# Kernel tuning notes

Hardware: AMD Instinct MI355X
Metric: run time of the kernel (lower is better)

## Reference

```python
import jax, jax.numpy as jnp
import numpy as np


def setup_inputs() -> dict:
    key = jax.random.key(0)
    k1, k2, k3, k4 = jax.random.split(key, 4)
    N, E, C_in, C_out = 50000, 625000, 256, 128
    x = jax.random.normal(k1, (N, C_in), dtype=jnp.float32)
    W = jax.random.normal(k2, (C_out, C_in), dtype=jnp.float32) * (1.0 / np.sqrt(C_in))
    b = jax.random.normal(k3, (C_out,), dtype=jnp.float32) * 0.01
    edge_index = jax.random.randint(k4, (2, E), 0, N, dtype=jnp.int64)
    return {"x": x, "W": W, "b": b, "edge_index": edge_index}


def reference(x, W, b, edge_index):
    # x: [N, C_in], W: [C_out, C_in], b: [C_out], edge_index: [2, E]
    N = x.shape[0]
    h = jnp.dot(x, W.T) + b  # [N, C_out] (nn.Linear)
    r, c = edge_index[0], edge_index[1]
    # node degree via scatter_add of ones over destination index r
    deg = jax.ops.segment_sum(jnp.ones(r.shape[0], dtype=h.dtype), r, num_segments=N)
    # rsqrt with inf (deg==0) replaced by 0
    nd_rsqrt = jnp.where(deg > 0, jax.lax.rsqrt(jnp.maximum(deg, 1.0)), jnp.zeros_like(deg))
    # gather messages from source nodes c, normalize by source rsqrt-degree
    message_norm = h[c] * nd_rsqrt[c][:, None]  # [E, C_out]
    # scatter-add to destination nodes r
    out = jax.ops.segment_sum(message_norm, r, num_segments=N)  # [N, C_out]
    # final destination-side normalization
    return out * nd_rsqrt[:, None]
```

## Files before the change

### kernel.cpp

```cpp
#include <hip/hip_runtime.h>

#define C_IN 256
#define C_OUT 128
#define ELL_PAD 64
#define NBUCKMAX 512
#define BNODE 128
#define BUCK_CAP 2048
#define EDGES_PER_BLK 4096
#define BLK 128

typedef __attribute__((ext_vector_type(8))) short bf16x8;
typedef __attribute__((ext_vector_type(8))) unsigned short ushort8;
typedef __attribute__((ext_vector_type(4))) float f32x4;

__device__ inline unsigned short f2bf(float f) {
    unsigned u = __builtin_bit_cast(unsigned, f);
    unsigned r = (u + 0x7FFFu + ((u >> 16) & 1u)) >> 16;
    return (unsigned short)r;
}
__device__ inline float bflo(unsigned u) { return __builtin_bit_cast(float, u << 16); }
__device__ inline float bfhi(unsigned u) { return __builtin_bit_cast(float, u & 0xFFFF0000u); }

__global__ __launch_bounds__(BLK) void wconv_zero_kernel(const float* __restrict__ W,
                                                         unsigned short* __restrict__ WB,
                                                         int* __restrict__ bucket_cnt) {
    int ci = blockIdx.x * BLK + threadIdx.x;
    int q = ci & 3, cl = (ci >> 2) & 15, ctt = ci >> 6;
    int colw = (ctt & 7) * 16 + cl;
    int k0 = (ctt >> 3) * 32 + q * 8;
    const float* src = W + colw * C_IN + k0;
    bf16x8 o;
    #pragma unroll
    for (int j = 0; j < 8; ++j) o[j] = (short)f2bf(src[j]);
    *(bf16x8*)(WB + (size_t)ci * 8) = o;
    if (ci < NBUCKMAX) bucket_cnt[ci] = 0;
}

__global__ __launch_bounds__(BLK) void fused_bucket_gemm(const float* __restrict__ x,
                                                         const unsigned short* __restrict__ WB,
                                                         const float* __restrict__ b,
                                                         const int* __restrict__ ridx,
                                                         const int* __restrict__ cidx,
                                                         int* __restrict__ bucket_cnt,
                                                         unsigned* __restrict__ buckets,
                                                         unsigned short* __restrict__ h,
                                                         int N, int E, int nbuck, int G_bkt) {
    __shared__ unsigned stage[EDGES_PER_BLK];
    __shared__ int cnt[NBUCKMAX];
    __shared__ int base[NBUCKMAX];
    __shared__ int off[NBUCKMAX];
    int t = threadIdx.x;

    int T = gridDim.x;
    long long i = blockIdx.x;
    int f_i  = (int)((i * (long long)G_bkt) / T);
    int f_i1 = (int)(((i + 1) * (long long)G_bkt) / T);

    if (f_i1 > f_i) {
        int e0 = f_i * EDGES_PER_BLK;
        int nv = E - e0; if (nv > EDGES_PER_BLK) nv = EDGES_PER_BLK;

        for (int bb = t; bb < NBUCKMAX; bb += BLK) { cnt[bb] = 0; off[bb] = 0; }
        __syncthreads();

        for (int k = t; k < nv; k += BLK) {
            int r = ridx[e0 + k];
            int c = cidx[e0 + k];
            stage[k] = ((unsigned)r << 16) | (unsigned)c;
            atomicAdd(&cnt[r >> 7], 1);
        }
        __syncthreads();

        for (int bb = t; bb < nbuck; bb += BLK) {
            int cb = cnt[bb];
            base[bb] = (cb > 0) ? atomicAdd(&bucket_cnt[bb], cb) : 0;
        }
        __syncthreads();

        for (int k = t; k < nv; k += BLK) {
            unsigned v = stage[k];
            int bkt = (int)(v >> 23);
            int p = atomicAdd(&off[bkt], 1);
            int dst = base[bkt] + p;
            if (dst < BUCK_CAP)
                buckets[(size_t)bkt * BUCK_CAP + dst] = v;
        }
        return;
    }

    int gemmId = (int)i - f_i;
    int w = t >> 6, l = t & 63;
    int row0 = gemmId * 32;
    int lq = l >> 4, lr = l & 15;

    int arow = row0 + w * 16 + lr;
    bool rowok = (arow < N);
    const float* xr = x + (size_t)(rowok ? arow : 0) * C_IN + lq * 8;
    const char* wb = (const char*)WB;
    int boff = lr * 64 + lq * 16;

    f32x4 acc[8];
    #pragma unroll
    for (int ct = 0; ct < 8; ++ct) acc[ct] = (f32x4){0.f, 0.f, 0.f, 0.f};

    #pragma unroll
    for (int tt = 0; tt < 8; ++tt) {
        float4 v0 = make_float4(0.f, 0.f, 0.f, 0.f);
        float4 v1 = make_float4(0.f, 0.f, 0.f, 0.f);
        if (rowok) {
            v0 = *(const float4*)(xr + tt * 32);
            v1 = *(const float4*)(xr + tt * 32 + 4);
        }
        bf16x8 af;
        af[0] = (short)f2bf(v0.x); af[1] = (short)f2bf(v0.y);
        af[2] = (short)f2bf(v0.z); af[3] = (short)f2bf(v0.w);
        af[4] = (short)f2bf(v1.x); af[5] = (short)f2bf(v1.y);
        af[6] = (short)f2bf(v1.z); af[7] = (short)f2bf(v1.w);
        #pragma unroll
        for (int ct = 0; ct < 8; ++ct) {
            bf16x8 bfv = *(const bf16x8*)(wb + (tt * 8 + ct) * 1024 + boff);
            acc[ct] = __builtin_amdgcn_mfma_f32_16x16x32_bf16(af, bfv, acc[ct], 0, 0, 0);
        }
    }

    #pragma unroll
    for (int ct = 0; ct < 8; ++ct) {
        int colc = ct * 16 + lr;
        float bv = b[colc];
        #pragma unroll
        for (int r = 0; r < 4; ++r) {
            int grow = row0 + w * 16 + lq * 4 + r;
            if (grow < N)
                h[(size_t)grow * C_OUT + colc] = f2bf(acc[ct][r] + bv);
        }
    }
}

__global__ __launch_bounds__(BLK) void build_ell_kernel(const int* __restrict__ bucket_cnt,
                                                        const unsigned* __restrict__ buckets,
                                                        int* __restrict__ deg,
                                                        float* __restrict__ s,
                                                        unsigned short* __restrict__ col_ell, int N) {
    __shared__ int cur[BNODE];
    __shared__ unsigned short ell[BNODE * ELL_PAD];
    int t = threadIdx.x;
    int b = blockIdx.x;
    cur[t] = 0;
    __syncthreads();

    int cnt = bucket_cnt[b];
    if (cnt > BUCK_CAP) cnt = BUCK_CAP;
    const unsigned* bb = buckets + (size_t)b * BUCK_CAP;
    for (int e = t; e < cnt; e += BLK) {
        unsigned v = bb[e];
        int rl = (v >> 16) & (BNODE - 1);
        int pos = atomicAdd(&cur[rl], 1);
        if (pos < ELL_PAD)
            ell[rl * ELL_PAD + pos] = (unsigned short)(v & 0xFFFFu);
    }
    __syncthreads();

    int node = b * BNODE + t;
    if (node < N) {
        int d = cur[t];
        deg[node] = d;
        s[node] = (d > 0) ? rsqrtf((float)d) : 0.0f;
        if (d > ELL_PAD) d = ELL_PAD;
        int chunks = (d + 7) >> 3;
        ushort8* dst = (ushort8*)(col_ell + (size_t)node * ELL_PAD);
        const ushort8* src = (const ushort8*)(ell + t * ELL_PAD);
        for (int j = 0; j < chunks; ++j) dst[j] = src[j];
    }
}

__global__ __launch_bounds__(BLK) void gather_kernel(const int* __restrict__ deg,
                                                     const float* __restrict__ s,
                                                     const unsigned short* __restrict__ col_ell,
                                                     const unsigned short* __restrict__ h,
                                                     float* __restrict__ out, int N) {
    int gid = blockIdx.x * BLK + threadIdx.x;
    int node = gid >> 4;
    if (node >= N) return;
    int lane = gid & 15;

    int d = deg[node];
    float sv = s[node];
    int dd = (d > ELL_PAD) ? ELL_PAD : d;
    const unsigned short* cl = col_ell + (size_t)node * ELL_PAD;
    const char* hb = (const char*)h;

    float acc[8] = {0.f, 0.f, 0.f, 0.f, 0.f, 0.f, 0.f, 0.f};
    int i = 0;
    for (; i + 4 <= dd; i += 4) {
        int c0 = cl[i], c1 = cl[i + 1], c2 = cl[i + 2], c3 = cl[i + 3];
        float s0 = s[c0], s1 = s[c1], s2 = s[c2], s3 = s[c3];
        uint4 v0 = *(const uint4*)(hb + (size_t)c0 * (C_OUT * 2) + lane * 16);
        uint4 v1 = *(const uint4*)(hb + (size_t)c1 * (C_OUT * 2) + lane * 16);
        uint4 v2 = *(const uint4*)(hb + (size_t)c2 * (C_OUT * 2) + lane * 16);
        uint4 v3 = *(const uint4*)(hb + (size_t)c3 * (C_OUT * 2) + lane * 16);
        acc[0] += s0 * bflo(v0.x); acc[1] += s0 * bfhi(v0.x);
        acc[2] += s0 * bflo(v0.y); acc[3] += s0 * bfhi(v0.y);
        acc[4] += s0 * bflo(v0.z); acc[5] += s0 * bfhi(v0.z);
        acc[6] += s0 * bflo(v0.w); acc[7] += s0 * bfhi(v0.w);
        acc[0] += s1 * bflo(v1.x); acc[1] += s1 * bfhi(v1.x);
        acc[2] += s1 * bflo(v1.y); acc[3] += s1 * bfhi(v1.y);
        acc[4] += s1 * bflo(v1.z); acc[5] += s1 * bfhi(v1.z);
        acc[6] += s1 * bflo(v1.w); acc[7] += s1 * bfhi(v1.w);
        acc[0] += s2 * bflo(v2.x); acc[1] += s2 * bfhi(v2.x);
        acc[2] += s2 * bflo(v2.y); acc[3] += s2 * bfhi(v2.y);
        acc[4] += s2 * bflo(v2.z); acc[5] += s2 * bfhi(v2.z);
        acc[6] += s2 * bflo(v2.w); acc[7] += s2 * bfhi(v2.w);
        acc[0] += s3 * bflo(v3.x); acc[1] += s3 * bfhi(v3.x);
        acc[2] += s3 * bflo(v3.y); acc[3] += s3 * bfhi(v3.y);
        acc[4] += s3 * bflo(v3.z); acc[5] += s3 * bfhi(v3.z);
        acc[6] += s3 * bflo(v3.w); acc[7] += s3 * bfhi(v3.w);
    }
    for (; i < dd; ++i) {
        int c0 = cl[i];
        float s0 = s[c0];
        uint4 v0 = *(const uint4*)(hb + (size_t)c0 * (C_OUT * 2) + lane * 16);
        acc[0] += s0 * bflo(v0.x); acc[1] += s0 * bfhi(v0.x);
        acc[2] += s0 * bflo(v0.y); acc[3] += s0 * bfhi(v0.y);
        acc[4] += s0 * bflo(v0.z); acc[5] += s0 * bfhi(v0.z);
        acc[6] += s0 * bflo(v0.w); acc[7] += s0 * bfhi(v0.w);
    }
    float4 o0 = make_float4(acc[0] * sv, acc[1] * sv, acc[2] * sv, acc[3] * sv);
    float4 o1 = make_float4(acc[4] * sv, acc[5] * sv, acc[6] * sv, acc[7] * sv);
    float* op = out + (size_t)node * C_OUT + lane * 8;
    *(float4*)(op)     = o0;
    *(float4*)(op + 4) = o1;
}

extern "C" void kernel_launch(void* const* d_in, const int* in_sizes, int n_in,
                              void* d_out, int out_size, void* d_ws, size_t ws_size,
                              hipStream_t stream) {
    const float* x = (const float*)d_in[0];
    const float* W = (const float*)d_in[1];
    const float* b = (const float*)d_in[2];
    const int*   ei = (const int*)d_in[3];
    float* out = (float*)d_out;

    int N = in_sizes[0] / C_IN;
    int E = in_sizes[3] / 2;
    const int* ridx = ei;
    const int* cidx = ei + E;

    int nbuck = (N + BNODE - 1) / BNODE;

    char* wsc = (char*)d_ws;
    unsigned short* h  = (unsigned short*)wsc;       wsc += (size_t)N * C_OUT * sizeof(unsigned short);
    unsigned short* WB = (unsigned short*)wsc;       wsc += (size_t)C_OUT * C_IN * sizeof(unsigned short);
    int*   deg      = (int*)wsc;                     wsc += (size_t)N * sizeof(int);
    float* s        = (float*)wsc;                   wsc += (size_t)N * sizeof(float);
    unsigned short* col_ell = (unsigned short*)wsc;  wsc += (size_t)N * ELL_PAD * sizeof(unsigned short);
    int*   bucket_cnt = (int*)wsc;                   wsc += (size_t)NBUCKMAX * sizeof(int);
    unsigned* buckets = (unsigned*)wsc;

    wconv_zero_kernel<<<4096 / BLK, BLK, 0, stream>>>(W, WB, bucket_cnt);

    int G_bkt  = (E + EDGES_PER_BLK - 1) / EDGES_PER_BLK;
    int G_gemm = (N + 31) / 32;
    fused_bucket_gemm<<<G_bkt + G_gemm, BLK, 0, stream>>>(x, WB, b, ridx, cidx,
                                                          bucket_cnt, buckets, h,
                                                          N, E, nbuck, G_bkt);

    build_ell_kernel<<<nbuck, BLK, 0, stream>>>(bucket_cnt, buckets, deg, s, col_ell, N);

    long long gth = (long long)N * 16;
    gather_kernel<<<(int)((gth + BLK - 1) / BLK), BLK, 0, stream>>>(deg, s, col_ell, h, out, N);
}
```

Before: 71.18 us.

## Split GEMM across bucket and ELL-build kernels; coalesce bucket writes via local sort

```diff
diff --git a/kernel.cpp b/kernel.cpp
--- a/kernel.cpp
+++ b/kernel.cpp
@@ -20,6 +20,57 @@
 }
 __device__ inline float bflo(unsigned u) { return __builtin_bit_cast(float, u << 16); }
 __device__ inline float bfhi(unsigned u) { return __builtin_bit_cast(float, u & 0xFFFF0000u); }
+
+__device__ __forceinline__ void gemm_unit(int gemmId, const float* __restrict__ x,
+                                          const unsigned short* __restrict__ WB,
+                                          const float* __restrict__ b,
+                                          unsigned short* __restrict__ h, int N, int t) {
+    int w = t >> 6, l = t & 63;
+    int row0 = gemmId * 32;
+    int lq = l >> 4, lr = l & 15;
+
+    int arow = row0 + w * 16 + lr;
+    bool rowok = (arow < N);
+    const float* xr = x + (size_t)(rowok ? arow : 0) * C_IN + lq * 8;
+    const char* wb = (const char*)WB;
+    int boff = lr * 64 + lq * 16;
+
+    f32x4 acc[8];
+    #pragma unroll
+    for (int ct = 0; ct < 8; ++ct) acc[ct] = (f32x4){0.f, 0.f, 0.f, 0.f};
+
+    #pragma unroll
+    for (int tt = 0; tt < 8; ++tt) {
+        float4 v0 = make_float4(0.f, 0.f, 0.f, 0.f);
+        float4 v1 = make_float4(0.f, 0.f, 0.f, 0.f);
+        if (rowok) {
+            v0 = *(const float4*)(xr + tt * 32);
+            v1 = *(const float4*)(xr + tt * 32 + 4);
+        }
+        bf16x8 af;
+        af[0] = (short)f2bf(v0.x); af[1] = (short)f2bf(v0.y);
+        af[2] = (short)f2bf(v0.z); af[3] = (short)f2bf(v0.w);
+        af[4] = (short)f2bf(v1.x); af[5] = (short)f2bf(v1.y);
+        af[6] = (short)f2bf(v1.z); af[7] = (short)f2bf(v1.w);
+        #pragma unroll
+        for (int ct = 0; ct < 8; ++ct) {
+            bf16x8 bfv = *(const bf16x8*)(wb + (tt * 8 + ct) * 1024 + boff);
+            acc[ct] = __builtin_amdgcn_mfma_f32_16x16x32_bf16(af, bfv, acc[ct], 0, 0, 0);
+        }
+    }
+
+    #pragma unroll
+    for (int ct = 0; ct < 8; ++ct) {
+        int colc = ct * 16 + lr;
+        float bv = b[colc];
+        #pragma unroll
+        for (int r = 0; r < 4; ++r) {
+            int grow = row0 + w * 16 + lq * 4 + r;
+            if (grow < N)
+                h[(size_t)grow * C_OUT + colc] = f2bf(acc[ct][r] + bv);
+        }
+    }
+}
 
 __global__ __launch_bounds__(BLK) void wconv_zero_kernel(const float* __restrict__ W,
                                                          unsigned short* __restrict__ WB,
@@ -36,19 +87,22 @@
     if (ci < NBUCKMAX) bucket_cnt[ci] = 0;
 }
 
-__global__ __launch_bounds__(BLK) void fused_bucket_gemm(const float* __restrict__ x,
-                                                         const unsigned short* __restrict__ WB,
-                                                         const float* __restrict__ b,
-                                                         const int* __restrict__ ridx,
-                                                         const int* __restrict__ cidx,
-                                                         int* __restrict__ bucket_cnt,
-                                                         unsigned* __restrict__ buckets,
-                                                         unsigned short* __restrict__ h,
-                                                         int N, int E, int nbuck, int G_bkt) {
+__global__ __launch_bounds__(BLK) void k1_bucket_gemm(const float* __restrict__ x,
+                                                      const unsigned short* __restrict__ WB,
+                                                      const float* __restrict__ b,
+                                                      const int* __restrict__ ridx,
+                                                      const int* __restrict__ cidx,
+                                                      int* __restrict__ bucket_cnt,
+                                                      unsigned* __restrict__ buckets,
+                                                      unsigned short* __restrict__ h,
+                                                      int N, int E, int nbuck, int G_bkt) {
     __shared__ unsigned stage[EDGES_PER_BLK];
+    __shared__ unsigned stage2[EDGES_PER_BLK];
     __shared__ int cnt[NBUCKMAX];
-    __shared__ int base[NBUCKMAX];
+    __shared__ int lbase[NBUCKMAX];
+    __shared__ int gbase[NBUCKMAX];
     __shared__ int off[NBUCKMAX];
+    __shared__ int part[BLK];
     int t = threadIdx.x;
 
     int T = gridDim.x;
@@ -60,6 +114,7 @@
         int e0 = f_i * EDGES_PER_BLK;
         int nv = E - e0; if (nv > EDGES_PER_BLK) nv = EDGES_PER_BLK;
 
+        #pragma unroll
         for (int bb = t; bb < NBUCKMAX; bb += BLK) { cnt[bb] = 0; off[bb] = 0; }
         __syncthreads();
 
@@ -71,9 +126,24 @@
         }
         __syncthreads();
 
-        for (int bb = t; bb < nbuck; bb += BLK) {
+        int c0 = cnt[4 * t], c1 = cnt[4 * t + 1], c2 = cnt[4 * t + 2], c3 = cnt[4 * t + 3];
+        part[t] = c0 + c1 + c2 + c3;
+        __syncthreads();
+        for (int o = 1; o < BLK; o <<= 1) {
+            int v = (t >= o) ? part[t - o] : 0;
+            __syncthreads();
+            part[t] += v;
+            __syncthreads();
+        }
+        int ex = (t > 0) ? part[t - 1] : 0;
+        lbase[4 * t]     = ex;
+        lbase[4 * t + 1] = ex + c0;
+        lbase[4 * t + 2] = ex + c0 + c1;
+        lbase[4 * t + 3] = ex + c0 + c1 + c2;
+        #pragma unroll
+        for (int bb = t; bb < NBUCKMAX; bb += BLK) {
             int cb = cnt[bb];
-            base[bb] = (cb > 0) ? atomicAdd(&bucket_cnt[bb], cb) : 0;
+            gbase[bb] = (cb > 0) ? atomicAdd(&bucket_cnt[bb], cb) : 0;
         }
         __syncthreads();
 
@@ -81,96 +151,74 @@
             unsigned v = stage[k];
             int bkt = (int)(v >> 23);
             int p = atomicAdd(&off[bkt], 1);
-            int dst = base[bkt] + p;
-            if (dst < BUCK_CAP)
-                buckets[(size_t)bkt * BUCK_CAP + dst] = v;
+            stage2[lbase[bkt] + p] = v;
+        }
+        __syncthreads();
+
+        for (int k = t; k < nv; k += BLK) {
+            unsigned v = stage2[k];
+            int bkt = (int)(v >> 23);
+            int gofs = gbase[bkt] + (k - lbase[bkt]);
+            if (gofs < BUCK_CAP)
+                buckets[(size_t)bkt * BUCK_CAP + gofs] = v;
         }
         return;
     }
 
-    int gemmId = (int)i - f_i;
-    int w = t >> 6, l = t & 63;
-    int row0 = gemmId * 32;
-    int lq = l >> 4, lr = l & 15;
-
-    int arow = row0 + w * 16 + lr;
-    bool rowok = (arow < N);
-    const float* xr = x + (size_t)(rowok ? arow : 0) * C_IN + lq * 8;
-    const char* wb = (const char*)WB;
-    int boff = lr * 64 + lq * 16;
-
-    f32x4 acc[8];
-    #pragma unroll
-    for (int ct = 0; ct < 8; ++ct) acc[ct] = (f32x4){0.f, 0.f, 0.f, 0.f};
-
-    #pragma unroll
-    for (int tt = 0; tt < 8; ++tt) {
-        float4 v0 = make_float4(0.f, 0.f, 0.f, 0.f);
-        float4 v1 = make_float4(0.f, 0.f, 0.f, 0.f);
-        if (rowok) {
-            v0 = *(const float4*)(xr + tt * 32);
-            v1 = *(const float4*)(xr + tt * 32 + 4);
-        }
-        bf16x8 af;
-        af[0] = (short)f2bf(v0.x); af[1] = (short)f2bf(v0.y);
-        af[2] = (short)f2bf(v0.z); af[3] = (short)f2bf(v0.w);
-        af[4] = (short)f2bf(v1.x); af[5] = (short)f2bf(v1.y);
-        af[6] = (short)f2bf(v1.z); af[7] = (short)f2bf(v1.w);
-        #pragma unroll
-        for (int ct = 0; ct < 8; ++ct) {
-            bf16x8 bfv = *(const bf16x8*)(wb + (tt * 8 + ct) * 1024 + boff);
-            acc[ct] = __builtin_amdgcn_mfma_f32_16x16x32_bf16(af, bfv, acc[ct], 0, 0, 0);
-        }
-    }
-
-    #pragma unroll
-    for (int ct = 0; ct < 8; ++ct) {
-        int colc = ct * 16 + lr;
-        float bv = b[colc];
-        #pragma unroll
-        for (int r = 0; r < 4; ++r) {
-            int grow = row0 + w * 16 + lq * 4 + r;
-            if (grow < N)
-                h[(size_t)grow * C_OUT + colc] = f2bf(acc[ct][r] + bv);
-        }
-    }
-}
-
-__global__ __launch_bounds__(BLK) void build_ell_kernel(const int* __restrict__ bucket_cnt,
-                                                        const unsigned* __restrict__ buckets,
-                                                        int* __restrict__ deg,
-                                                        float* __restrict__ s,
-                                                        unsigned short* __restrict__ col_ell, int N) {
+    gemm_unit((int)i - f_i, x, WB, b, h, N, t);
+}
+
+__global__ __launch_bounds__(BLK) void k2_build_gemm(const float* __restrict__ x,
+                                                     const unsigned short* __restrict__ WB,
+                                                     const float* __restrict__ b,
+                                                     const int* __restrict__ bucket_cnt,
+                                                     const unsigned* __restrict__ buckets,
+                                                     int* __restrict__ deg,
+                                                     float* __restrict__ s,
+                                                     unsigned short* __restrict__ col_ell,
+                                                     unsigned short* __restrict__ h,
+                                                     int N, int nbuck, int G1) {
     __shared__ int cur[BNODE];
     __shared__ unsigned short ell[BNODE * ELL_PAD];
     int t = threadIdx.x;
-    int b = blockIdx.x;
-    cur[t] = 0;
-    __syncthreads();
-
-    int cnt = bucket_cnt[b];
-    if (cnt > BUCK_CAP) cnt = BUCK_CAP;
-    const unsigned* bb = buckets + (size_t)b * BUCK_CAP;
-    for (int e = t; e < cnt; e += BLK) {
-        unsigned v = bb[e];
-        int rl = (v >> 16) & (BNODE - 1);
-        int pos = atomicAdd(&cur[rl], 1);
-        if (pos < ELL_PAD)
-            ell[rl * ELL_PAD + pos] = (unsigned short)(v & 0xFFFFu);
-    }
-    __syncthreads();
-
-    int node = b * BNODE + t;
-    if (node < N) {
-        int d = cur[t];
-        deg[node] = d;
-        s[node] = (d > 0) ? rsqrtf((float)d) : 0.0f;
-        if (d > ELL_PAD) d = ELL_PAD;
-        int chunks = (d + 7) >> 3;
-        ushort8* dst = (ushort8*)(col_ell + (size_t)node * ELL_PAD);
-        const ushort8* src = (const ushort8*)(ell + t * ELL_PAD);
-        for (int j = 0; j < chunks; ++j) dst[j] = src[j];
-    }
+
+    int T = gridDim.x;
+    long long i = blockIdx.x;
+    int f_i  = (int)((i * (long long)nbuck) / T);
+    int f_i1 = (int)(((i + 1) * (long long)nbuck) / T);
+
+    if (f_i1 > f_i) {
+        int bkt = f_i;
+        cur[t] = 0;
+        __syncthreads();
+
+        int cnt = bucket_cnt[bkt];
+        if (cnt > BUCK_CAP) cnt = BUCK_CAP;
+        const unsigned* bb = buckets + (size_t)bkt * BUCK_CAP;
+        for (int e = t; e < cnt; e += BLK) {
+            unsigned v = bb[e];
+            int rl = (v >> 16) & (BNODE - 1);
+            int pos = atomicAdd(&cur[rl], 1);
+            if (pos < ELL_PAD)
+                ell[rl * ELL_PAD + pos] = (unsigned short)(v & 0xFFFFu);
+        }
+        __syncthreads();
+
+        int node = bkt * BNODE + t;
+        if (node < N) {
+            int d = cur[t];
+            deg[node] = d;
+            s[node] = (d > 0) ? rsqrtf((float)d) : 0.0f;
+            if (d > ELL_PAD) d = ELL_PAD;
+            int chunks = (d + 7) >> 3;
+            ushort8* dst = (ushort8*)(col_ell + (size_t)node * ELL_PAD);
+            const ushort8* src = (const ushort8*)(ell + t * ELL_PAD);
+            for (int j = 0; j < chunks; ++j) dst[j] = src[j];
+        }
+        return;
+    }
+
+    gemm_unit(G1 + ((int)i - f_i), x, WB, b, h, N, t);
 }
 
 __global__ __launch_bounds__(BLK) void gather_kernel(const int* __restrict__ deg,
@@ -258,13 +306,17 @@
 
     wconv_zero_kernel<<<4096 / BLK, BLK, 0, stream>>>(W, WB, bucket_cnt);
 
-    int G_bkt  = (E + EDGES_PER_BLK - 1) / EDGES_PER_BLK;
-    int G_gemm = (N + 31) / 32;
-    fused_bucket_gemm<<<G_bkt + G_gemm, BLK, 0, stream>>>(x, WB, b, ridx, cidx,
-                                                          bucket_cnt, buckets, h,
-                                                          N, E, nbuck, G_bkt);
-
-    build_ell_kernel<<<nbuck, BLK, 0, stream>>>(bucket_cnt, buckets, deg, s, col_ell, N);
+    int G_bkt   = (E + EDGES_PER_BLK - 1) / EDGES_PER_BLK;
+    int G_gemmT = (N + 31) / 32;
+    int G1 = G_gemmT / 2;
+    int G2 = G_gemmT - G1;
+
+    k1_bucket_gemm<<<G_bkt + G1, BLK, 0, stream>>>(x, WB, b, ridx, cidx,
+                                                   bucket_cnt, buckets, h,
+                                                   N, E, nbuck, G_bkt);
+
+    k2_build_gemm<<<nbuck + G2, BLK, 0, stream>>>(x, WB, b, bucket_cnt, buckets,
+                                                  deg, s, col_ell, h, N, nbuck, G1);
 
     long long gth = (long long)N * 16;
     gather_kernel<<<(int)((gth + BLK - 1) / BLK), BLK, 0, stream>>>(deg, s, col_ell, h, out, N);
```

New measurement: 88.76 us. 1.25x slower.

## Locally sort edges by bucket in LDS before coalesced bucket writes

Applied to the files above, without the earlier changes.

```diff
diff --git a/kernel.cpp b/kernel.cpp
--- a/kernel.cpp
+++ b/kernel.cpp
@@ -6,7 +6,7 @@
 #define NBUCKMAX 512
 #define BNODE 128
 #define BUCK_CAP 2048
-#define EDGES_PER_BLK 4096
+#define EDGES_PER_BLK 2048
 #define BLK 128
 
 typedef __attribute__((ext_vector_type(8))) short bf16x8;
@@ -20,6 +20,12 @@
 }
 __device__ inline float bflo(unsigned u) { return __builtin_bit_cast(float, u << 16); }
 __device__ inline float bfhi(unsigned u) { return __builtin_bit_cast(float, u & 0xFFFF0000u); }
+
+#define ACC8(sv, vv)                                              \
+    acc[0] += sv * bflo(vv.x); acc[1] += sv * bfhi(vv.x);         \
+    acc[2] += sv * bflo(vv.y); acc[3] += sv * bfhi(vv.y);         \
+    acc[4] += sv * bflo(vv.z); acc[5] += sv * bfhi(vv.z);         \
+    acc[6] += sv * bflo(vv.w); acc[7] += sv * bfhi(vv.w);
 
 __global__ __launch_bounds__(BLK) void wconv_zero_kernel(const float* __restrict__ W,
                                                          unsigned short* __restrict__ WB,
@@ -46,9 +52,12 @@
                                                          unsigned short* __restrict__ h,
                                                          int N, int E, int nbuck, int G_bkt) {
     __shared__ unsigned stage[EDGES_PER_BLK];
+    __shared__ unsigned stage2[EDGES_PER_BLK];
     __shared__ int cnt[NBUCKMAX];
-    __shared__ int base[NBUCKMAX];
+    __shared__ int lbase[NBUCKMAX];
+    __shared__ int gbase[NBUCKMAX];
     __shared__ int off[NBUCKMAX];
+    __shared__ int part[BLK];
     int t = threadIdx.x;
 
     int T = gridDim.x;
@@ -60,6 +69,7 @@
         int e0 = f_i * EDGES_PER_BLK;
         int nv = E - e0; if (nv > EDGES_PER_BLK) nv = EDGES_PER_BLK;
 
+        #pragma unroll
         for (int bb = t; bb < NBUCKMAX; bb += BLK) { cnt[bb] = 0; off[bb] = 0; }
         __syncthreads();
 
@@ -71,9 +81,24 @@
         }
         __syncthreads();
 
-        for (int bb = t; bb < nbuck; bb += BLK) {
+        int c0 = cnt[4 * t], c1 = cnt[4 * t + 1], c2 = cnt[4 * t + 2], c3 = cnt[4 * t + 3];
+        part[t] = c0 + c1 + c2 + c3;
+        __syncthreads();
+        for (int o = 1; o < BLK; o <<= 1) {
+            int v = (t >= o) ? part[t - o] : 0;
+            __syncthreads();
+            part[t] += v;
+            __syncthreads();
+        }
+        int ex = (t > 0) ? part[t - 1] : 0;
+        lbase[4 * t]     = ex;
+        lbase[4 * t + 1] = ex + c0;
+        lbase[4 * t + 2] = ex + c0 + c1;
+        lbase[4 * t + 3] = ex + c0 + c1 + c2;
+        #pragma unroll
+        for (int bb = t; bb < NBUCKMAX; bb += BLK) {
             int cb = cnt[bb];
-            base[bb] = (cb > 0) ? atomicAdd(&bucket_cnt[bb], cb) : 0;
+            gbase[bb] = (cb > 0) ? atomicAdd(&bucket_cnt[bb], cb) : 0;
         }
         __syncthreads();
 
@@ -81,9 +106,16 @@
             unsigned v = stage[k];
             int bkt = (int)(v >> 23);
             int p = atomicAdd(&off[bkt], 1);
-            int dst = base[bkt] + p;
-            if (dst < BUCK_CAP)
-                buckets[(size_t)bkt * BUCK_CAP + dst] = v;
+            stage2[lbase[bkt] + p] = v;
+        }
+        __syncthreads();
+
+        for (int k = t; k < nv; k += BLK) {
+            unsigned v = stage2[k];
+            int bkt = (int)(v >> 23);
+            int gofs = gbase[bkt] + (k - lbase[bkt]);
+            if (gofs < BUCK_CAP)
+                buckets[(size_t)bkt * BUCK_CAP + gofs] = v;
         }
         return;
     }
@@ -198,31 +230,13 @@
         uint4 v1 = *(const uint4*)(hb + (size_t)c1 * (C_OUT * 2) + lane * 16);
         uint4 v2 = *(const uint4*)(hb + (size_t)c2 * (C_OUT * 2) + lane * 16);
         uint4 v3 = *(const uint4*)(hb + (size_t)c3 * (C_OUT * 2) + lane * 16);
-        acc[0] += s0 * bflo(v0.x); acc[1] += s0 * bfhi(v0.x);
-        acc[2] += s0 * bflo(v0.y); acc[3] += s0 * bfhi(v0.y);
-        acc[4] += s0 * bflo(v0.z); acc[5] += s0 * bfhi(v0.z);
-        acc[6] += s0 * bflo(v0.w); acc[7] += s0 * bfhi(v0.w);
-        acc[0] += s1 * bflo(v1.x); acc[1] += s1 * bfhi(v1.x);
-        acc[2] += s1 * bflo(v1.y); acc[3] += s1 * bfhi(v1.y);
-        acc[4] += s1 * bflo(v1.z); acc[5] += s1 * bfhi(v1.z);
-        acc[6] += s1 * bflo(v1.w); acc[7] += s1 * bfhi(v1.w);
-        acc[0] += s2 * bflo(v2.x); acc[1] += s2 * bfhi(v2.x);
-        acc[2] += s2 * bflo(v2.y); acc[3] += s2 * bfhi(v2.y);
-        acc[4] += s2 * bflo(v2.z); acc[5] += s2 * bfhi(v2.z);
-        acc[6] += s2 * bflo(v2.w); acc[7] += s2 * bfhi(v2.w);
-        acc[0] += s3 * bflo(v3.x); acc[1] += s3 * bfhi(v3.x);
-        acc[2] += s3 * bflo(v3.y); acc[3] += s3 * bfhi(v3.y);
-        acc[4] += s3 * bflo(v3.z); acc[5] += s3 * bfhi(v3.z);
-        acc[6] += s3 * bflo(v3.w); acc[7] += s3 * bfhi(v3.w);
+        ACC8(s0, v0) ACC8(s1, v1) ACC8(s2, v2) ACC8(s3, v3)
     }
     for (; i < dd; ++i) {
         int c0 = cl[i];
         float s0 = s[c0];
         uint4 v0 = *(const uint4*)(hb + (size_t)c0 * (C_OUT * 2) + lane * 16);
-        acc[0] += s0 * bflo(v0.x); acc[1] += s0 * bfhi(v0.x);
-        acc[2] += s0 * bflo(v0.y); acc[3] += s0 * bfhi(v0.y);
-        acc[4] += s0 * bflo(v0.z); acc[5] += s0 * bfhi(v0.z);
-        acc[6] += s0 * bflo(v0.w); acc[7] += s0 * bfhi(v0.w);
+        ACC8(s0, v0)
     }
     float4 o0 = make_float4(acc[0] * sv, acc[1] * sv, acc[2] * sv, acc[3] * sv);
     float4 o1 = make_float4(acc[4] * sv, acc[5] * sv, acc[6] * sv, acc[7] * sv);
```

Measured after the change: 84.35 us. +18.5%, slower.
